# Kernel tuning notes

Hardware: AMD Instinct MI355X
Metric: run time of the kernel (lower is better)

## Reference

```python
import jax, jax.numpy as jnp
import numpy as np

D_MODEL = 1024
N_HEAD = 16
SEQ = 2048
BATCH = 2


def setup_inputs() -> dict:
    key = jax.random.key(0)
    x = jax.random.normal(key, (BATCH, SEQ, D_MODEL), dtype=jnp.float32)
    return {"x": x}


def reference(x) -> jnp.ndarray:
    B, S, D = x.shape
    H = N_HEAD
    hd = D // H
    # split heads: q=k=v=x -> [B, H, S, hd]
    qkv = x.reshape(B, S, H, hd).transpose(0, 2, 1, 3)
    q = k = v = qkv
    # scores [B, H, S, S], scaled by sqrt(head_dim)
    w = jnp.einsum("bhqd,bhkd->bhqk", q, k) / jnp.sqrt(jnp.asarray(hd, x.dtype))
    # causal mask (nd == ns == S here)
    causal = jnp.tril(jnp.ones((S, S), dtype=bool))
    mask_value = jnp.finfo(w.dtype).min
    w = jnp.where(causal[None, None, :, :], w, mask_value)
    w = jax.nn.softmax(w, axis=-1)
    out = jnp.einsum("bhqk,bhkd->bhqd", w, v)
    # merge heads -> [B, S, D]
    return out.transpose(0, 2, 1, 3).reshape(B, S, D)
```

## Files before the change

kernel.cpp:

```cpp
#include <hip/hip_runtime.h>
#include <hip/hip_bf16.h>

#define BATCH  2
#define SEQ    2048
#define DMODEL 1024
#define NHEAD  16
#define HD     64
#define BH     (BATCH * NHEAD)

typedef __attribute__((ext_vector_type(8))) short s8v;
typedef __attribute__((ext_vector_type(16))) float f16v;

#define QK_BETA 0.42466089f

__device__ inline unsigned short bf16_rne(float f) {
    unsigned u = __builtin_bit_cast(unsigned, f);
    u += 0x7FFFu + ((u >> 16) & 1u);
    return (unsigned short)(u >> 16);
}

__device__ __forceinline__ unsigned pk_bf16(float lo, float hi) {
    __hip_bfloat162 h = __float22bfloat162_rn(make_float2(lo, hi));
    unsigned u;
    __builtin_memcpy(&u, &h, 4);
    return u;
}

__global__ __launch_bounds__(256) void prep_kernel(const float* __restrict__ x,
                                                   unsigned short* __restrict__ xb,
                                                   unsigned short* __restrict__ xbT) {
    __shared__ unsigned short tileT[64 * 40];
    const int id = blockIdx.x;
    const int bh = id & (BH - 1);
    const int st = id >> 5;
    const int b = bh >> 4, h = bh & (NHEAD - 1);
    const int s0 = st * 32;
    const int tid = threadIdx.x;
    const int c4 = tid & 15, r16 = tid >> 4;

    const size_t off0 = (size_t)(b * SEQ + s0 + r16) * DMODEL + h * HD + c4 * 4;
    const size_t off1 = (size_t)(b * SEQ + s0 + 16 + r16) * DMODEL + h * HD + c4 * 4;
    const float4 v0 = *(const float4*)(x + off0);
    const float4 v1 = *(const float4*)(x + off1);

    {
        uint2 u;
        u.x = pk_bf16(v0.x * QK_BETA, v0.y * QK_BETA);
        u.y = pk_bf16(v0.z * QK_BETA, v0.w * QK_BETA);
        *(uint2*)(xb + off0) = u;
        u.x = pk_bf16(v1.x * QK_BETA, v1.y * QK_BETA);
        u.y = pk_bf16(v1.z * QK_BETA, v1.w * QK_BETA);
        *(uint2*)(xb + off1) = u;
    }
    {
        const int d0 = c4 * 4;
        unsigned short* t0 = tileT + r16;
        t0[(d0 + 0) * 40] = bf16_rne(v0.x);
        t0[(d0 + 1) * 40] = bf16_rne(v0.y);
        t0[(d0 + 2) * 40] = bf16_rne(v0.z);
        t0[(d0 + 3) * 40] = bf16_rne(v0.w);
        unsigned short* t1 = tileT + 16 + r16;
        t1[(d0 + 0) * 40] = bf16_rne(v1.x);
        t1[(d0 + 1) * 40] = bf16_rne(v1.y);
        t1[(d0 + 2) * 40] = bf16_rne(v1.z);
        t1[(d0 + 3) * 40] = bf16_rne(v1.w);
    }
    __syncthreads();
    {
        const int d = tid >> 2;
        const int sq = (tid & 3) * 8;
        const s8v o = *(const s8v*)(tileT + d * 40 + sq);
        *(s8v*)(xbT + (size_t)(bh * HD + d) * SEQ + s0 + sq) = o;
    }
}

__device__ __forceinline__ void stage_tile(const unsigned short* __restrict__ xbh,
                                           const unsigned short* __restrict__ xTh,
                                           char* lds, int bufoff, int k0,
                                           int w, int sr, int sc) {
    if (w < 2) {
#pragma unroll
        for (int i = 0; i < 4; ++i) {
            const int r = w * 32 + i * 8 + sr;
            const unsigned short* gsrc =
                xbh + (size_t)(k0 + r) * DMODEL + ((sc ^ (r & 7)) * 8);
            const int loff = __builtin_amdgcn_readfirstlane(bufoff + (w * 32 + i * 8) * 128);
            __builtin_amdgcn_global_load_lds(
                (const __attribute__((address_space(1))) void*)gsrc,
                (__attribute__((address_space(3))) void*)(lds + loff), 16, 0, 0);
        }
    } else {
#pragma unroll
        for (int i = 0; i < 4; ++i) {
            const int d = (w - 2) * 32 + i * 8 + sr;
            const unsigned short* gsrc =
                xTh + (size_t)d * SEQ + k0 + ((sc ^ (d & 7)) * 8);
            const int loff =
                __builtin_amdgcn_readfirstlane(bufoff + 8192 + ((w - 2) * 32 + i * 8) * 128);
            __builtin_amdgcn_global_load_lds(
                (const __attribute__((address_space(1))) void*)gsrc,
                (__attribute__((address_space(3))) void*)(lds + loff), 16, 0, 0);
        }
    }
}

__global__ __launch_bounds__(256, 2) void flash_kernel(const unsigned short* __restrict__ xb,
                                                       const unsigned short* __restrict__ xbT,
                                                       float* __restrict__ out) {
    __shared__ __align__(16) char lds[49152];

    const int id = blockIdx.x;
    const int bh = id & (BH - 1);
    const int j = id >> 5;
    const int qt = (j < 8) ? (15 - j) : (j - 8);
    const int b = bh >> 4, h = bh & (NHEAD - 1);
    const int tid = threadIdx.x;
    const int w = tid >> 6;
    const int lane = tid & 63;
    const int qh = lane & 31;
    const int hh = lane >> 5;
    const int qbase = qt * 128;

    const unsigned short* xbh = xb + (size_t)b * SEQ * DMODEL + h * HD;
    const unsigned short* xTh = xbT + (size_t)bh * HD * SEQ;

    const int qrow = qbase + w * 32 + qh;
    s8v qf0 = *(const s8v*)(xbh + (size_t)qrow * DMODEL + 0 * 16 + hh * 8);
    s8v qf1 = *(const s8v*)(xbh + (size_t)qrow * DMODEL + 1 * 16 + hh * 8);
    s8v qf2 = *(const s8v*)(xbh + (size_t)qrow * DMODEL + 2 * 16 + hh * 8);
    s8v qf3 = *(const s8v*)(xbh + (size_t)qrow * DMODEL + 3 * 16 + hh * 8);

    int kbo[2][4];
    int vbo[2][4];
#pragma unroll
    for (int i2 = 0; i2 < 2; ++i2)
#pragma unroll
        for (int c = 0; c < 4; ++c) {
            kbo[i2][c] = (i2 * 32 + qh) * 128 + (((2 * c + hh) ^ (qh & 7)) * 16);
            vbo[i2][c] = 8192 + (i2 * 32 + qh) * 128 + (((2 * c + hh) ^ (qh & 7)) * 16);
        }

    char* const Pbase = lds + 32768 + w * 4096;
    int pwo0[4], pwo1[4], pro[4];
#pragma unroll
    for (int j2 = 0; j2 < 4; ++j2) {
        pwo0[j2] = qh * 128 + (((j2 + 0) ^ (qh & 7)) * 16) + 8 * hh;
        pwo1[j2] = qh * 128 + (((j2 + 4) ^ (qh & 7)) * 16) + 8 * hh;
        pro[j2]  = qh * 128 + (((2 * j2 + hh) ^ (qh & 7)) * 16);
    }

    f16v o0 = {0,0,0,0,0,0,0,0,0,0,0,0,0,0,0,0};
    f16v o1 = o0;
    float lsum = 0.0f;

    const int sr = lane >> 3;
    const int sc = lane & 7;

    stage_tile(xbh, xTh, lds, 0, 0, w, sr, sc);

    const int ktEnd = 2 * qt + 1;
    for (int kt = 0; kt <= ktEnd; ++kt) {
        char* const buf = lds + ((kt & 1) << 14);
        __syncthreads();
        if (kt < ktEnd)
            stage_tile(xbh, xTh, lds, ((kt & 1) ^ 1) << 14, (kt + 1) * 64, w, sr, sc);

        const int base_off = qbase + w * 32 - kt * 64;
        if (base_off + 31 < 0) continue;
        const bool fullLive = (base_off >= 63);
        const int qlim = base_off + qh;

        f16v c0 = {0,0,0,0,0,0,0,0,0,0,0,0,0,0,0,0};
        f16v c1 = c0;
        __builtin_amdgcn_s_setprio(1);
        c0 = __builtin_amdgcn_mfma_f32_32x32x16_bf16(*(const s8v*)(buf + kbo[0][0]), qf0, c0, 0, 0, 0);
        c0 = __builtin_amdgcn_mfma_f32_32x32x16_bf16(*(const s8v*)(buf + kbo[0][1]), qf1, c0, 0, 0, 0);
        c0 = __builtin_amdgcn_mfma_f32_32x32x16_bf16(*(const s8v*)(buf + kbo[0][2]), qf2, c0, 0, 0, 0);
        c0 = __builtin_amdgcn_mfma_f32_32x32x16_bf16(*(const s8v*)(buf + kbo[0][3]), qf3, c0, 0, 0, 0);
        c1 = __builtin_amdgcn_mfma_f32_32x32x16_bf16(*(const s8v*)(buf + kbo[1][0]), qf0, c1, 0, 0, 0);
        c1 = __builtin_amdgcn_mfma_f32_32x32x16_bf16(*(const s8v*)(buf + kbo[1][1]), qf1, c1, 0, 0, 0);
        c1 = __builtin_amdgcn_mfma_f32_32x32x16_bf16(*(const s8v*)(buf + kbo[1][2]), qf2, c1, 0, 0, 0);
        c1 = __builtin_amdgcn_mfma_f32_32x32x16_bf16(*(const s8v*)(buf + kbo[1][3]), qf3, c1, 0, 0, 0);
        __builtin_amdgcn_s_setprio(0);

        float p0[16], p1[16];
#pragma unroll
        for (int e = 0; e < 16; ++e) {
            p0[e] = __builtin_amdgcn_exp2f(c0[e]);
            p1[e] = __builtin_amdgcn_exp2f(c1[e]);
        }
        if (!fullLive) {
#pragma unroll
            for (int e = 0; e < 16; ++e) {
                const int kl = (e & 3) + 8 * (e >> 2) + 4 * hh;
                p0[e] = (kl <= qlim) ? p0[e] : 0.0f;
                p1[e] = (kl + 32 <= qlim) ? p1[e] : 0.0f;
            }
        }
#pragma unroll
        for (int e = 0; e < 16; ++e) lsum += p0[e] + p1[e];
#pragma unroll
        for (int j2 = 0; j2 < 4; ++j2) {
            uint2 u;
            u.x = pk_bf16(p0[4 * j2 + 0], p0[4 * j2 + 1]);
            u.y = pk_bf16(p0[4 * j2 + 2], p0[4 * j2 + 3]);
            *(uint2*)(Pbase + pwo0[j2]) = u;
            u.x = pk_bf16(p1[4 * j2 + 0], p1[4 * j2 + 1]);
            u.y = pk_bf16(p1[4 * j2 + 2], p1[4 * j2 + 3]);
            *(uint2*)(Pbase + pwo1[j2]) = u;
        }

        const s8v pa0 = *(const s8v*)(Pbase + pro[0]);
        const s8v pa1 = *(const s8v*)(Pbase + pro[1]);
        const s8v pa2 = *(const s8v*)(Pbase + pro[2]);
        const s8v pa3 = *(const s8v*)(Pbase + pro[3]);
        __builtin_amdgcn_s_setprio(1);
        o0 = __builtin_amdgcn_mfma_f32_32x32x16_bf16(pa0, *(const s8v*)(buf + vbo[0][0]), o0, 0, 0, 0);
        o1 = __builtin_amdgcn_mfma_f32_32x32x16_bf16(pa0, *(const s8v*)(buf + vbo[1][0]), o1, 0, 0, 0);
        o0 = __builtin_amdgcn_mfma_f32_32x32x16_bf16(pa1, *(const s8v*)(buf + vbo[0][1]), o0, 0, 0, 0);
        o1 = __builtin_amdgcn_mfma_f32_32x32x16_bf16(pa1, *(const s8v*)(buf + vbo[1][1]), o1, 0, 0, 0);
        o0 = __builtin_amdgcn_mfma_f32_32x32x16_bf16(pa2, *(const s8v*)(buf + vbo[0][2]), o0, 0, 0, 0);
        o1 = __builtin_amdgcn_mfma_f32_32x32x16_bf16(pa2, *(const s8v*)(buf + vbo[1][2]), o1, 0, 0, 0);
        o0 = __builtin_amdgcn_mfma_f32_32x32x16_bf16(pa3, *(const s8v*)(buf + vbo[0][3]), o0, 0, 0, 0);
        o1 = __builtin_amdgcn_mfma_f32_32x32x16_bf16(pa3, *(const s8v*)(buf + vbo[1][3]), o1, 0, 0, 0);
        __builtin_amdgcn_s_setprio(0);
    }

    lsum += __shfl_xor(lsum, 32, 64);
    float invr[16];
#pragma unroll
    for (int e = 0; e < 16; ++e) {
        const int rowq = (e & 3) + 8 * (e >> 2) + 4 * hh;
        invr[e] = 1.0f / __shfl(lsum, rowq, 64);
    }

    float* outh = out + (size_t)b * SEQ * DMODEL + h * HD;
#pragma unroll
    for (int e = 0; e < 16; ++e) {
        const int rowq = (e & 3) + 8 * (e >> 2) + 4 * hh;
        const size_t ro = (size_t)(qbase + w * 32 + rowq) * DMODEL;
        outh[ro + 0 * 32 + qh] = o0[e] * invr[e];
        outh[ro + 1 * 32 + qh] = o1[e] * invr[e];
    }
}

#define KT 32
#define QR 16
#define LDS_STRIDE 68

__global__ __launch_bounds__(64, 2)
void attn_fp32_kernel(const float* __restrict__ x, float* __restrict__ out) {
    __shared__ float kv[KT * LDS_STRIDE];
    const int id = blockIdx.x;
    const int bh = id & (BATCH * NHEAD - 1);
    const int qt = (SEQ / QR - 1) - (id >> 5);
    const int b = bh >> 4, h = bh & (NHEAD - 1);
    const int lane = threadIdx.x;
    const int row = lane & (QR - 1);
    const int slice = lane >> 4;
    const int qrow = qt * QR + row;
    const float* xh = x + (size_t)b * SEQ * DMODEL + (size_t)h * HD;
    float q[HD], o[HD];
    const float4* qp = (const float4*)(xh + (size_t)qrow * DMODEL);
#pragma unroll
    for (int i = 0; i < HD / 4; ++i) {
        float4 v = qp[i];
        q[4*i+0] = v.x * 0.125f; q[4*i+1] = v.y * 0.125f;
        q[4*i+2] = v.z * 0.125f; q[4*i+3] = v.w * 0.125f;
    }
#pragma unroll
    for (int d = 0; d < HD; ++d) o[d] = 0.0f;
    float l = 0.0f;
    const int kend = qt * QR + QR;
    for (int kt0 = 0; kt0 < kend; kt0 += KT) {
        __syncthreads();
#pragma unroll
        for (int i = 0; i < (KT * HD / 4) / 64; ++i) {
            int idx = i * 64 + lane;
            int r = idx >> 4, cc = idx & 15;
            *(float4*)(kv + r * LDS_STRIDE + cc * 4) =
                *(const float4*)(xh + (size_t)(kt0 + r) * DMODEL + cc * 4);
        }
        __syncthreads();
#pragma unroll 2
        for (int jj = 0; jj < KT / 4; ++jj) {
            const int j = jj * 4 + slice;
            const float* kr = kv + j * LDS_STRIDE;
            float a0 = 0.f, a1 = 0.f, a2 = 0.f, a3 = 0.f;
#pragma unroll
            for (int dq = 0; dq < 16; ++dq) {
                float4 kk = ((const float4*)kr)[dq];
                a0 = fmaf(q[4*dq+0], kk.x, a0); a1 = fmaf(q[4*dq+1], kk.y, a1);
                a2 = fmaf(q[4*dq+2], kk.z, a2); a3 = fmaf(q[4*dq+3], kk.w, a3);
            }
            float p = __expf((a0 + a1) + (a2 + a3));
            p = (kt0 + j <= qrow) ? p : 0.0f;
            l += p;
#pragma unroll
            for (int dq = 0; dq < 16; ++dq) {
                float4 vv = ((const float4*)kr)[dq];
                o[4*dq+0] = fmaf(p, vv.x, o[4*dq+0]); o[4*dq+1] = fmaf(p, vv.y, o[4*dq+1]);
                o[4*dq+2] = fmaf(p, vv.z, o[4*dq+2]); o[4*dq+3] = fmaf(p, vv.w, o[4*dq+3]);
            }
        }
    }
    l += __shfl_xor(l, 16, 64);
    l += __shfl_xor(l, 32, 64);
#pragma unroll
    for (int d = 0; d < HD; ++d) {
        o[d] += __shfl_xor(o[d], 16, 64);
        o[d] += __shfl_xor(o[d], 32, 64);
    }
    if (slice == 0) {
        const float invl = 1.0f / l;
        float4* op = (float4*)(out + ((size_t)b * SEQ + qrow) * DMODEL + (size_t)h * HD);
#pragma unroll
        for (int i = 0; i < HD / 4; ++i) {
            float4 v;
            v.x = o[4*i+0] * invl; v.y = o[4*i+1] * invl;
            v.z = o[4*i+2] * invl; v.w = o[4*i+3] * invl;
            op[i] = v;
        }
    }
}

extern "C" void kernel_launch(void* const* d_in, const int* in_sizes, int n_in,
                              void* d_out, int out_size, void* d_ws, size_t ws_size,
                              hipStream_t stream) {
    const float* x = (const float*)d_in[0];
    float* out = (float*)d_out;
    const size_t nXb = (size_t)BATCH * SEQ * DMODEL;
    const size_t need = 2 * nXb * 2;
    if (ws_size >= need) {
        unsigned short* xb  = (unsigned short*)d_ws;
        unsigned short* xbT = xb + nXb;
        hipLaunchKernelGGL(prep_kernel, dim3(BH * SEQ / 32), dim3(256), 0, stream,
                           x, xb, xbT);
        hipLaunchKernelGGL(flash_kernel, dim3(BH * SEQ / 128), dim3(256), 0, stream,
                           xb, xbT, out);
    } else {
        hipLaunchKernelGGL(attn_fp32_kernel, dim3(BATCH * NHEAD * (SEQ / QR)), dim3(64), 0,
                           stream, x, out);
    }
}
```

Before: 106.5 us.

## Use 64-row query tiles with 2 waves and permlane P transpose

Query tiles shrink from 128 to 64 rows, so blocks drop from 4 to 2 waves and the grid doubles, using a new heavy/light interleaving of tile order. Each wave now stages a full K or V tile. The bf16 P matrix is rearranged into the MFMA A-operand layout in registers using v_permlane32_swap instead of a round trip through LDS, which removes the P scratch buffer and cuts LDS to 32 KB. This removes LDS traffic and a dead-tile skip branch, but each block reloads K/V for fewer queries and per-wave staging work doubles.

```diff
diff --git a/kernel.cpp b/kernel.cpp
--- a/kernel.cpp
+++ b/kernel.cpp
@@ -10,6 +10,7 @@
 
 typedef __attribute__((ext_vector_type(8))) short s8v;
 typedef __attribute__((ext_vector_type(16))) float f16v;
+typedef __attribute__((ext_vector_type(4))) unsigned u4v;
 
 #define QK_BETA 0.42466089f
 
@@ -24,6 +25,10 @@
     unsigned u;
     __builtin_memcpy(&u, &h, 4);
     return u;
+}
+
+__device__ __forceinline__ void pl32swap(unsigned& a, unsigned& b) {
+    asm volatile("v_permlane32_swap_b32 %0, %1" : "+v"(a), "+v"(b));
 }
 
 __global__ __launch_bounds__(256) void prep_kernel(const float* __restrict__ x,
@@ -74,29 +79,28 @@
     }
 }
 
-__device__ __forceinline__ void stage_tile(const unsigned short* __restrict__ xbh,
-                                           const unsigned short* __restrict__ xTh,
-                                           char* lds, int bufoff, int k0,
-                                           int w, int sr, int sc) {
-    if (w < 2) {
-#pragma unroll
-        for (int i = 0; i < 4; ++i) {
-            const int r = w * 32 + i * 8 + sr;
+__device__ __forceinline__ void stage_tile2(const unsigned short* __restrict__ xbh,
+                                            const unsigned short* __restrict__ xTh,
+                                            char* lds, int bufoff, int k0,
+                                            int w, int sr, int sc) {
+    if (w == 0) {
+#pragma unroll
+        for (int i = 0; i < 8; ++i) {
+            const int r = i * 8 + sr;
             const unsigned short* gsrc =
                 xbh + (size_t)(k0 + r) * DMODEL + ((sc ^ (r & 7)) * 8);
-            const int loff = __builtin_amdgcn_readfirstlane(bufoff + (w * 32 + i * 8) * 128);
+            const int loff = __builtin_amdgcn_readfirstlane(bufoff + i * 1024);
             __builtin_amdgcn_global_load_lds(
                 (const __attribute__((address_space(1))) void*)gsrc,
                 (__attribute__((address_space(3))) void*)(lds + loff), 16, 0, 0);
         }
     } else {
 #pragma unroll
-        for (int i = 0; i < 4; ++i) {
-            const int d = (w - 2) * 32 + i * 8 + sr;
+        for (int i = 0; i < 8; ++i) {
+            const int d = i * 8 + sr;
             const unsigned short* gsrc =
                 xTh + (size_t)d * SEQ + k0 + ((sc ^ (d & 7)) * 8);
-            const int loff =
-                __builtin_amdgcn_readfirstlane(bufoff + 8192 + ((w - 2) * 32 + i * 8) * 128);
+            const int loff = __builtin_amdgcn_readfirstlane(bufoff + 8192 + i * 1024);
             __builtin_amdgcn_global_load_lds(
                 (const __attribute__((address_space(1))) void*)gsrc,
                 (__attribute__((address_space(3))) void*)(lds + loff), 16, 0, 0);
@@ -104,34 +108,35 @@
     }
 }
 
-__global__ __launch_bounds__(256, 2) void flash_kernel(const unsigned short* __restrict__ xb,
+__global__ __launch_bounds__(128, 2) void flash_kernel(const unsigned short* __restrict__ xb,
                                                        const unsigned short* __restrict__ xbT,
                                                        float* __restrict__ out) {
-    __shared__ __align__(16) char lds[49152];
+    __shared__ __align__(16) char lds[32768];
 
     const int id = blockIdx.x;
     const int bh = id & (BH - 1);
-    const int j = id >> 5;
-    const int qt = (j < 8) ? (15 - j) : (j - 8);
+    const int t5 = id >> 5;
+    const int rr = t5 >> 3, uu = t5 & 7;
+    const int qt = (rr == 0) ? (31 - uu) : (rr == 1) ? (16 + uu)
+                 : (rr == 2) ? (15 - uu) : uu;
     const int b = bh >> 4, h = bh & (NHEAD - 1);
     const int tid = threadIdx.x;
     const int w = tid >> 6;
     const int lane = tid & 63;
     const int qh = lane & 31;
     const int hh = lane >> 5;
-    const int qbase = qt * 128;
+    const int qbase = qt * 64;
 
     const unsigned short* xbh = xb + (size_t)b * SEQ * DMODEL + h * HD;
     const unsigned short* xTh = xbT + (size_t)bh * HD * SEQ;
 
     const int qrow = qbase + w * 32 + qh;
-    s8v qf0 = *(const s8v*)(xbh + (size_t)qrow * DMODEL + 0 * 16 + hh * 8);
-    s8v qf1 = *(const s8v*)(xbh + (size_t)qrow * DMODEL + 1 * 16 + hh * 8);
-    s8v qf2 = *(const s8v*)(xbh + (size_t)qrow * DMODEL + 2 * 16 + hh * 8);
-    s8v qf3 = *(const s8v*)(xbh + (size_t)qrow * DMODEL + 3 * 16 + hh * 8);
-
-    int kbo[2][4];
-    int vbo[2][4];
+    const s8v qf0 = *(const s8v*)(xbh + (size_t)qrow * DMODEL + 0 * 16 + hh * 8);
+    const s8v qf1 = *(const s8v*)(xbh + (size_t)qrow * DMODEL + 1 * 16 + hh * 8);
+    const s8v qf2 = *(const s8v*)(xbh + (size_t)qrow * DMODEL + 2 * 16 + hh * 8);
+    const s8v qf3 = *(const s8v*)(xbh + (size_t)qrow * DMODEL + 3 * 16 + hh * 8);
+
+    int kbo[2][4], vbo[2][4];
 #pragma unroll
     for (int i2 = 0; i2 < 2; ++i2)
 #pragma unroll
@@ -140,15 +145,6 @@
             vbo[i2][c] = 8192 + (i2 * 32 + qh) * 128 + (((2 * c + hh) ^ (qh & 7)) * 16);
         }
 
-    char* const Pbase = lds + 32768 + w * 4096;
-    int pwo0[4], pwo1[4], pro[4];
-#pragma unroll
-    for (int j2 = 0; j2 < 4; ++j2) {
-        pwo0[j2] = qh * 128 + (((j2 + 0) ^ (qh & 7)) * 16) + 8 * hh;
-        pwo1[j2] = qh * 128 + (((j2 + 4) ^ (qh & 7)) * 16) + 8 * hh;
-        pro[j2]  = qh * 128 + (((2 * j2 + hh) ^ (qh & 7)) * 16);
-    }
-
     f16v o0 = {0,0,0,0,0,0,0,0,0,0,0,0,0,0,0,0};
     f16v o1 = o0;
     float lsum = 0.0f;
@@ -156,17 +152,15 @@
     const int sr = lane >> 3;
     const int sc = lane & 7;
 
-    stage_tile(xbh, xTh, lds, 0, 0, w, sr, sc);
-
-    const int ktEnd = 2 * qt + 1;
-    for (int kt = 0; kt <= ktEnd; ++kt) {
+    stage_tile2(xbh, xTh, lds, 0, 0, w, sr, sc);
+
+    for (int kt = 0; kt <= qt; ++kt) {
         char* const buf = lds + ((kt & 1) << 14);
         __syncthreads();
-        if (kt < ktEnd)
-            stage_tile(xbh, xTh, lds, ((kt & 1) ^ 1) << 14, (kt + 1) * 64, w, sr, sc);
+        if (kt < qt)
+            stage_tile2(xbh, xTh, lds, ((kt & 1) ^ 1) << 14, (kt + 1) * 64, w, sr, sc);
 
         const int base_off = qbase + w * 32 - kt * 64;
-        if (base_off + 31 < 0) continue;
         const bool fullLive = (base_off >= 63);
         const int qlim = base_off + qh;
 
@@ -199,21 +193,30 @@
         }
 #pragma unroll
         for (int e = 0; e < 16; ++e) lsum += p0[e] + p1[e];
-#pragma unroll
-        for (int j2 = 0; j2 < 4; ++j2) {
-            uint2 u;
-            u.x = pk_bf16(p0[4 * j2 + 0], p0[4 * j2 + 1]);
-            u.y = pk_bf16(p0[4 * j2 + 2], p0[4 * j2 + 3]);
-            *(uint2*)(Pbase + pwo0[j2]) = u;
-            u.x = pk_bf16(p1[4 * j2 + 0], p1[4 * j2 + 1]);
-            u.y = pk_bf16(p1[4 * j2 + 2], p1[4 * j2 + 3]);
-            *(uint2*)(Pbase + pwo1[j2]) = u;
-        }
-
-        const s8v pa0 = *(const s8v*)(Pbase + pro[0]);
-        const s8v pa1 = *(const s8v*)(Pbase + pro[1]);
-        const s8v pa2 = *(const s8v*)(Pbase + pro[2]);
-        const s8v pa3 = *(const s8v*)(Pbase + pro[3]);
+
+        unsigned u0[8], u1[8];
+#pragma unroll
+        for (int m = 0; m < 8; ++m) {
+            u0[m] = pk_bf16(p0[2 * m], p0[2 * m + 1]);
+            u1[m] = pk_bf16(p1[2 * m], p1[2 * m + 1]);
+        }
+        u4v pw0, pw1, pw2, pw3;
+        {
+            unsigned a, b2;
+            a = u0[0]; b2 = u0[2]; pl32swap(a, b2); pw0[0] = a; pw0[2] = b2;
+            a = u0[1]; b2 = u0[3]; pl32swap(a, b2); pw0[1] = a; pw0[3] = b2;
+            a = u0[4]; b2 = u0[6]; pl32swap(a, b2); pw1[0] = a; pw1[2] = b2;
+            a = u0[5]; b2 = u0[7]; pl32swap(a, b2); pw1[1] = a; pw1[3] = b2;
+            a = u1[0]; b2 = u1[2]; pl32swap(a, b2); pw2[0] = a; pw2[2] = b2;
+            a = u1[1]; b2 = u1[3]; pl32swap(a, b2); pw2[1] = a; pw2[3] = b2;
+            a = u1[4]; b2 = u1[6]; pl32swap(a, b2); pw3[0] = a; pw3[2] = b2;
+            a = u1[5]; b2 = u1[7]; pl32swap(a, b2); pw3[1] = a; pw3[3] = b2;
+        }
+        const s8v pa0 = __builtin_bit_cast(s8v, pw0);
+        const s8v pa1 = __builtin_bit_cast(s8v, pw1);
+        const s8v pa2 = __builtin_bit_cast(s8v, pw2);
+        const s8v pa3 = __builtin_bit_cast(s8v, pw3);
+
         __builtin_amdgcn_s_setprio(1);
         o0 = __builtin_amdgcn_mfma_f32_32x32x16_bf16(pa0, *(const s8v*)(buf + vbo[0][0]), o0, 0, 0, 0);
         o1 = __builtin_amdgcn_mfma_f32_32x32x16_bf16(pa0, *(const s8v*)(buf + vbo[1][0]), o1, 0, 0, 0);
@@ -336,7 +339,7 @@
         unsigned short* xbT = xb + nXb;
         hipLaunchKernelGGL(prep_kernel, dim3(BH * SEQ / 32), dim3(256), 0, stream,
                            x, xb, xbT);
-        hipLaunchKernelGGL(flash_kernel, dim3(BH * SEQ / 128), dim3(256), 0, stream,
+        hipLaunchKernelGGL(flash_kernel, dim3(BH * SEQ / 64), dim3(128), 0, stream,
                            xb, xbT, out);
     } else {
         hipLaunchKernelGGL(attn_fp32_kernel, dim3(BATCH * NHEAD * (SEQ / QR)), dim3(64), 0,
```

New measurement: 104.8 us. Within noise of the previous version (-1.5%).
